# Kernel optimization log

Measured on AMD Instinct MI355X. Metric: run time of the kernel, lower is better.

The kernel has to match this reference:

```python
import jax, jax.numpy as jnp
import numpy as np

# dims
B, L, HID = 2, 1024, 2048
NH, HD, NKV = 32, 64, 8
INTER = 8192
DSSM, MH, MP, MS, MG, MK = 2048, 32, 64, 64, 1, 4
CONV_DIM = DSSM + 2 * MG * MS
EPS = 1e-5
ROPE_BASE = 1e11
# multipliers from config
KEY_MULT, ATTN_IN, ATTN_OUT = 0.7, 1.2, 0.8
SSM_IN, SSM_OUT = 1.1, 0.9
GATE_MULT, DOWN_MULT = 0.9, 0.8
SSM_MULTS = (1.0, 0.9, 0.8, 1.1, 1.2)


def _rms(x, w, eps=EPS):
    return x * jax.lax.rsqrt(jnp.mean(x * x, -1, keepdims=True) + eps) * w


def _rope(pos, x):  # neox-style, full head_dim; x: (B,L,H,HD)
    half = HD // 2
    inv = ROPE_BASE ** (-jnp.arange(0, HD, 2, dtype=jnp.float32) / HD)
    ang = pos.astype(jnp.float32)[:, None] * inv  # (L, half)
    cos = jnp.cos(ang)[None, :, None, :]
    sin = jnp.sin(ang)[None, :, None, :]
    x1, x2 = x[..., :half], x[..., half:]
    return jnp.concatenate([x1 * cos - x2 * sin, x2 * cos + x1 * sin], -1)


def _mup_vector():
    return jnp.concatenate([
        jnp.full((DSSM,), SSM_MULTS[0], jnp.float32),
        jnp.full((DSSM,), SSM_MULTS[1], jnp.float32),
        jnp.full((MG * MS,), SSM_MULTS[2], jnp.float32),
        jnp.full((MG * MS,), SSM_MULTS[3], jnp.float32),
        jnp.full((MH,), SSM_MULTS[4], jnp.float32),
    ])


def setup_inputs() -> dict:
    key = jax.random.key(0)
    ks = jax.random.split(key, 16)
    s = 0.02
    return {
        "hidden_states": jax.random.normal(ks[0], (B, L, HID), jnp.float32),
        "positions": jnp.arange(L, dtype=jnp.int32),
        "w_in_ln": jnp.ones((HID,), jnp.float32),
        "qkv_w": jax.random.normal(ks[1], (NH * HD + 2 * NKV * HD, HID), jnp.float32) * s,
        "o_w": jax.random.normal(ks[2], (HID, NH * HD), jnp.float32) * s,
        "in_proj_w": jax.random.normal(ks[3], (2 * DSSM + 2 * MG * MS + MH, HID), jnp.float32) * s,
        "conv_w": jax.random.normal(ks[4], (CONV_DIM, MK), jnp.float32) * 0.1,
        "conv_b": jax.random.normal(ks[5], (CONV_DIM,), jnp.float32) * 0.01,
        "A_log": jnp.log(jnp.linspace(1.0, 16.0, MH, dtype=jnp.float32)),
        "dt_bias": jax.random.normal(ks[6], (MH,), jnp.float32) * 0.1,
        "D": jnp.ones((MH,), jnp.float32),
        "ssm_norm_w": jnp.ones((DSSM,), jnp.float32),
        "out_proj_w": jax.random.normal(ks[7], (HID, DSSM), jnp.float32) * s,
        "w_pre_ff_ln": jnp.ones((HID,), jnp.float32),
        "gate_up_w": jax.random.normal(ks[8], (2 * INTER, HID), jnp.float32) * s,
        "down_w": jax.random.normal(ks[9], (HID, INTER), jnp.float32) * s,
    }


def _attention(hs, positions, qkv_w, o_w):
    qkv = hs @ qkv_w.T
    qs, kvs = NH * HD, NKV * HD
    q = qkv[..., :qs].reshape(B, L, NH, HD)
    k = qkv[..., qs:qs + kvs].reshape(B, L, NKV, HD) * KEY_MULT
    v = qkv[..., qs + kvs:].reshape(B, L, NKV, HD)
    q = _rope(positions, q)
    k = _rope(positions, k)
    rep = NH // NKV
    qg = q.reshape(B, L, NKV, rep, HD)
    scores = jnp.einsum('blgrd,bmgd->bgrlm', qg, k) * (HD ** -0.5)
    mask = jnp.tril(jnp.ones((L, L), bool))
    scores = jnp.where(mask[None, None, None], scores, jnp.float32(-1e9))
    attn = jax.nn.softmax(scores, axis=-1)
    out = jnp.einsum('bgrlm,bmgd->blgrd', attn, v).reshape(B, L, NH * HD)
    return out @ o_w.T


def _mamba(hs, in_proj_w, conv_w, conv_b, A_log, dt_bias, D, ssm_norm_w, out_proj_w):
    proj = (hs @ in_proj_w.T) * _mup_vector()  # (B,L,2*DSSM+2*G*S+MH)
    z = proj[..., :DSSM]
    xBC = proj[..., DSSM:DSSM + CONV_DIM]
    dt = proj[..., -MH:]
    # causal depthwise conv1d, kernel MK, then silu
    xpad = jnp.pad(xBC, ((0, 0), (MK - 1, 0), (0, 0)))
    conv = sum(xpad[:, k:k + L, :] * conv_w[:, k] for k in range(MK)) + conv_b
    xBC = jax.nn.silu(conv)
    x = xBC[..., :DSSM].reshape(B, L, MH, MP)
    Bm = xBC[..., DSSM:DSSM + MG * MS].reshape(B, L, MS)  # G=1
    C = xBC[..., DSSM + MG * MS:].reshape(B, L, MS)
    dt = jax.nn.softplus(dt + dt_bias)  # (B,L,MH)
    A = -jnp.exp(A_log)  # (MH,)

    def step(state, inp):  # state: (B,MH,MP,MS)
        x_t, dt_t, b_t, c_t = inp  # (B,MH,MP),(B,MH),(B,MS),(B,MS)
        dA = jnp.exp(dt_t * A)  # (B,MH)
        dBx = dt_t[..., None, None] * x_t[..., None] * b_t[:, None, None, :]
        state = state * dA[..., None, None] + dBx
        y = jnp.einsum('bhps,bs->bhp', state, c_t)
        return state, y

    xs = (jnp.moveaxis(x, 1, 0), jnp.moveaxis(dt, 1, 0),
          jnp.moveaxis(Bm, 1, 0), jnp.moveaxis(C, 1, 0))
    state0 = jnp.zeros((B, MH, MP, MS), hs.dtype)
    _, ys = jax.lax.scan(step, state0, xs)
    y = jnp.moveaxis(ys, 0, 1) + x * D[None, None, :, None]  # (B,L,MH,MP)
    y = y.reshape(B, L, DSSM)
    # gated RMSNorm: gate with silu(z), then rms-normalize
    g = y * jax.nn.silu(z)
    g = _rms(g, ssm_norm_w)
    return g @ out_proj_w.T


def _mlp(x, gate_up_w, down_w):
    gu = x @ gate_up_w.T
    gate = gu[..., :INTER] * GATE_MULT
    up = gu[..., INTER:]
    return (jax.nn.silu(gate) * up) @ down_w.T * DOWN_MULT


def reference(hidden_states, positions, w_in_ln, qkv_w, o_w, in_proj_w, conv_w,
              conv_b, A_log, dt_bias, D, ssm_norm_w, out_proj_w, w_pre_ff_ln,
              gate_up_w, down_w):
    residual = hidden_states
    hs = _rms(hidden_states, w_in_ln)
    attn_h = _attention(hs * ATTN_IN, positions, qkv_w, o_w)
    ssm_h = _mamba(hs * SSM_IN, in_proj_w, conv_w, conv_b, A_log, dt_bias, D,
                   ssm_norm_w, out_proj_w)
    h = attn_h * ATTN_OUT + ssm_h * SSM_OUT + residual
    residual = h
    h = _rms(h, w_pre_ff_ln)
    h = _mlp(h, gate_up_w, down_w)
    return h + residual
```

## Files before the change

### kernel.cpp

```cpp
#include <hip/hip_runtime.h>
#include <hip/hip_bf16.h>
#include <math.h>

#define B_      2
#define L_      1024
#define HID     2048
#define T_      (B_*L_)
#define NH      32
#define HD      64
#define NKV     8
#define INTER   8192
#define DSSM    2048
#define MH      32
#define MP      64
#define MS      64
#define MK      4
#define CONV_DIM 2176
#define QKV_N   3072
#define INPROJ_N 4256
#define CH      16
#define CL      64

typedef __bf16 bf16x8 __attribute__((ext_vector_type(8)));
typedef __bf16 bf16x4 __attribute__((ext_vector_type(4)));
typedef float  floatx4 __attribute__((ext_vector_type(4)));

static const size_t OFF_H2   = 0;
static const size_t OFF_MUP  = 4194304;
static const size_t AR       = 4210688;
static const size_t OFF_WQKV = AR;
static const size_t OFF_WIN  = OFF_WQKV + 3145728;
static const size_t OFF_WO   = OFF_WIN  + 4358144;
static const size_t OFF_WOP  = OFF_WO   + 2097152;
static const size_t OFF_HSB  = OFF_WOP  + 2097152;
static const size_t OFF_HSF  = OFF_HSB  + 2097152;
static const size_t OFF_QKV  = OFF_HSF  + 4194304;
static const size_t OFF_Q    = OFF_QKV  + 6291456;
static const size_t OFF_K    = OFF_Q    + 2097152;
static const size_t OFF_V    = OFF_K    + 524288;
static const size_t OFF_ATT  = OFF_V    + 524288;
static const size_t OFF_PROJ = OFF_ATT  + 2097152;
static const size_t OFF_XBC  = OFF_PROJ + 8716288;
static const size_t OFF_Y    = OFF_XBC  + 4456448;
static const size_t OFF_G    = OFF_Y    + 4194304;
static const size_t OFF_TB   = OFF_QKV;
static const size_t OFF_DEC  = OFF_Q;
static const size_t OFF_LAM  = OFF_V;
static const size_t OFF_HS2B = AR;
static const size_t OFF_GU   = AR + 2097152;
static const size_t OFF_ACTB = OFF_GU + 33554432;
static const size_t OFF_WB2  = OFF_ACTB + 8388608;

__device__ inline float block_sum(float v, float* red) {
#pragma unroll
  for (int o = 32; o > 0; o >>= 1) v += __shfl_down(v, o, 64);
  const int lane = threadIdx.x & 63, wv = threadIdx.x >> 6;
  if (lane == 0) red[wv] = v;
  __syncthreads();
  if (threadIdx.x == 0) red[0] = red[0] + red[1] + red[2] + red[3];
  __syncthreads();
  float r = red[0];
  __syncthreads();
  return r;
}

__device__ inline bf16x8 pack8(float4 a, float4 b, float scale) {
  bf16x8 v;
  v[0] = (__bf16)(a.x * scale); v[1] = (__bf16)(a.y * scale);
  v[2] = (__bf16)(a.z * scale); v[3] = (__bf16)(a.w * scale);
  v[4] = (__bf16)(b.x * scale); v[5] = (__bf16)(b.y * scale);
  v[6] = (__bf16)(b.z * scale); v[7] = (__bf16)(b.w * scale);
  return v;
}

__device__ __forceinline__ void async16(const void* g, void* l) {
  __builtin_amdgcn_global_load_lds(
      (const __attribute__((address_space(1))) void*)g,
      (__attribute__((address_space(3))) void*)l, 16, 0, 0);
}

__global__ __launch_bounds__(256) void cvt_kernel(
    const float* __restrict__ in, __bf16* __restrict__ outp, int n8)
{
  int i = blockIdx.x * 256 + threadIdx.x;
  const int stride = gridDim.x * 256;
  for (; i < n8; i += stride) {
    const float4* p = (const float4*)(in + (size_t)i * 8);
    float4 a = p[0], b = p[1];
    bf16x8 v;
    v[0] = (__bf16)a.x; v[1] = (__bf16)a.y; v[2] = (__bf16)a.z; v[3] = (__bf16)a.w;
    v[4] = (__bf16)b.x; v[5] = (__bf16)b.y; v[6] = (__bf16)b.z; v[7] = (__bf16)b.w;
    *(bf16x8*)(outp + (size_t)i * 8) = v;
  }
}

__global__ __launch_bounds__(256) void copy_kernel(
    const float* __restrict__ in, float* __restrict__ outp)
{
  const size_t i = ((size_t)blockIdx.x * 256 + threadIdx.x) * 4;
  *(float4*)&outp[i] = *(const float4*)&in[i];
}

__global__ __launch_bounds__(256) void gemm_bf_kernel(
    const __bf16* __restrict__ A, const __bf16* __restrict__ W,
    float* __restrict__ out, const float* __restrict__ addin,
    const float* __restrict__ colscale,
    int N, int K, int ldo, float alpha)
{
  __shared__ __align__(16) __bf16 As[128 * 32];
  __shared__ __align__(16) __bf16 Bs[128 * 32];
  const int tid = threadIdx.x;
  const int lane = tid & 63, wave = tid >> 6;
  const int fr = lane & 15, fq = lane >> 4;
  const int m0 = blockIdx.x * 128, n0 = blockIdx.y * 128;
  const int wm = (wave >> 1) * 64, wn = (wave & 1) * 64;

  const int KS = K / gridDim.z;
  const int kbase = blockIdx.z * KS;

  const int srow = wave * 32 + (lane >> 2);
  const int selem = (lane & 3) * 8;
  const __bf16* ga0 = A + (size_t)(m0 + srow) * K + kbase + selem;
  const __bf16* ga1 = ga0 + (size_t)16 * K;
  int wr0 = n0 + srow;      if (wr0 >= N) wr0 = N - 1;
  int wr1 = n0 + srow + 16; if (wr1 >= N) wr1 = N - 1;
  const __bf16* gb0 = W + (size_t)wr0 * K + kbase + selem;
  const __bf16* gb1 = W + (size_t)wr1 * K + kbase + selem;
  __bf16* lA0 = &As[(wave * 2 + 0) * 512];
  __bf16* lA1 = &As[(wave * 2 + 1) * 512];
  __bf16* lB0 = &Bs[(wave * 2 + 0) * 512];
  __bf16* lB1 = &Bs[(wave * 2 + 1) * 512];

  floatx4 acc[4][4];
#pragma unroll
  for (int i = 0; i < 4; i++)
#pragma unroll
    for (int j = 0; j < 4; j++) acc[i][j] = (floatx4){0.f, 0.f, 0.f, 0.f};

  for (int kk = 0; kk < KS; kk += 32) {
    async16(ga0, lA0); async16(ga1, lA1);
    async16(gb0, lB0); async16(gb1, lB1);
    ga0 += 32; ga1 += 32; gb0 += 32; gb1 += 32;
    __syncthreads();

    bf16x8 aF[4], bF[4];
#pragma unroll
    for (int i = 0; i < 4; i++)
      aF[i] = *(const bf16x8*)&As[(wm + i * 16 + fr) * 32 + fq * 8];
#pragma unroll
    for (int j = 0; j < 4; j++)
      bF[j] = *(const bf16x8*)&Bs[(wn + j * 16 + fr) * 32 + fq * 8];
#pragma unroll
    for (int i = 0; i < 4; i++)
#pragma unroll
      for (int j = 0; j < 4; j++)
        acc[i][j] = __builtin_amdgcn_mfma_f32_16x16x32_bf16(aF[i], bF[j], acc[i][j], 0, 0, 0);
    __syncthreads();
  }

  const bool at = (gridDim.z > 1);
#pragma unroll
  for (int i = 0; i < 4; i++) {
#pragma unroll
    for (int r = 0; r < 4; r++) {
      const int m = m0 + wm + i * 16 + fq * 4 + r;
      float* orow = out + (size_t)m * ldo;
      const float* arow = addin ? (addin + (size_t)m * ldo) : nullptr;
#pragma unroll
      for (int j = 0; j < 4; j++) {
        const int n = n0 + wn + j * 16 + fr;
        if (n < N) {
          float vv = acc[i][j][r] * alpha;
          if (colscale) vv *= colscale[n];
          if (at) {
            atomicAdd(&orow[n], vv);
          } else {
            if (arow) vv += arow[n];
            orow[n] = vv;
          }
        }
      }
    }
  }
}

__global__ __launch_bounds__(256) void rms_kernel(
    const float* __restrict__ in, const float* __restrict__ w,
    __bf16* __restrict__ outb, float* __restrict__ outf, float* __restrict__ copy)
{
  __shared__ float buf[HID];
  __shared__ float red[8];
  const int tid = threadIdx.x;
  const size_t t = blockIdx.x;
  const float* row = in + t * HID;
  float ss = 0.f;
  for (int i = tid; i < HID; i += 256) { float x = row[i]; buf[i] = x; ss += x * x; }
  float tot = block_sum(ss, red);
  float inv = rsqrtf(tot / (float)HID + 1e-5f);
  for (int i = tid; i < HID; i += 256) {
    float x = buf[i];
    float val = x * inv * w[i];
    outb[t * HID + i] = (__bf16)val;
    if (outf) outf[t * HID + i] = val;
    if (copy) copy[t * HID + i] = x;
  }
}

__global__ void mup_kernel(float* __restrict__ mup) {
  int i = blockIdx.x * 256 + threadIdx.x;
  if (i >= INPROJ_N) return;
  float v = (i < DSSM) ? 1.0f
          : (i < 2 * DSSM) ? 0.9f
          : (i < 2 * DSSM + MS) ? 0.8f
          : (i < 2 * DSSM + 2 * MS) ? 1.1f
          : 1.2f;
  mup[i] = v;
}

__global__ __launch_bounds__(256) void rope_kernel(
    const float* __restrict__ qkv, const int* __restrict__ positions,
    __bf16* __restrict__ q, __bf16* __restrict__ k, __bf16* __restrict__ v)
{
  __shared__ float inv_s[32];
  const int tid = threadIdx.x;
  const size_t t = blockIdx.x;
  const int l = (int)(t & (L_ - 1));
  if (tid < 32) inv_s[tid] = powf(1.0e11f, -(float)(2 * tid) / 64.f);
  __syncthreads();
  const float pos = (float)positions[l];
  const float* src = qkv + t * QKV_N;
  for (int idx = tid; idx < 1536; idx += 256) {
    int head = idx >> 5, hd = idx & 31;
    if (head < 32) {
      float ang = pos * inv_s[hd];
      float c = cosf(ang), sn = sinf(ang);
      float x1 = src[head * 64 + hd], x2 = src[head * 64 + 32 + hd];
      __bf16* dst = q + (t * NH + head) * HD;
      dst[hd] = (__bf16)((x1 * c - x2 * sn) * 0.125f);
      dst[hd + 32] = (__bf16)((x2 * c + x1 * sn) * 0.125f);
    } else if (head < 40) {
      int kk = head - 32;
      float ang = pos * inv_s[hd];
      float c = cosf(ang), sn = sinf(ang);
      float x1 = src[2048 + kk * 64 + hd] * 0.7f;
      float x2 = src[2048 + kk * 64 + 32 + hd] * 0.7f;
      __bf16* dst = k + (t * NKV + kk) * HD;
      dst[hd] = (__bf16)(x1 * c - x2 * sn);
      dst[hd + 32] = (__bf16)(x2 * c + x1 * sn);
    } else {
      int vv = head - 40;
      __bf16* dst = v + (t * NKV + vv) * HD;
      dst[hd] = (__bf16)src[2560 + vv * 64 + hd];
      dst[hd + 32] = (__bf16)src[2560 + vv * 64 + 32 + hd];
    }
  }
}

__global__ __launch_bounds__(256) void fattn_kernel(
    const __bf16* __restrict__ q, const __bf16* __restrict__ k,
    const __bf16* __restrict__ v, __bf16* __restrict__ out)
{
  __shared__ __align__(16) __bf16 Vt[64][72];
  __shared__ __align__(16) __bf16 Ps[4][16][72];
  const int tid = threadIdx.x;
  const int wave = tid >> 6, lane = tid & 63;
  const int fr = lane & 15, fq = lane >> 4;
  const int qt = (int)(gridDim.x - 1) - blockIdx.x;
  const int h = blockIdx.y, b = blockIdx.z, g = h >> 2;
  const int l0 = qt * 64;

  bf16x8 qf[2];
  {
    const int qrow = l0 + wave * 16 + fr;
    const __bf16* qp = q + (((size_t)(b * L_ + qrow)) * NH + h) * HD;
    qf[0] = *(const bf16x8*)&qp[fq * 8];
    qf[1] = *(const bf16x8*)&qp[32 + fq * 8];
  }

  floatx4 O[4];
  float m_run[4], l_run[4];
#pragma unroll
  for (int i = 0; i < 4; i++) { O[i] = (floatx4){0.f,0.f,0.f,0.f}; m_run[i] = -3.0e38f; l_run[i] = 0.f; }

  for (int kt = 0; kt <= qt; kt++) {
    __syncthreads();
#pragma unroll
    for (int pp = 0; pp < 4; pp++) {
      const int kb = pp * 4 + wave;
      bf16x4 pk;
#pragma unroll
      for (int c = 0; c < 4; c++)
        pk[c] = v[(((size_t)(b * L_ + kt * 64 + kb * 4 + c)) * NKV + g) * HD + lane];
      *(bf16x4*)&Vt[lane][kb * 4] = pk;
    }

    floatx4 S[4];
#pragma unroll
    for (int j = 0; j < 4; j++) {
      const __bf16* kp = k + (((size_t)(b * L_ + kt * 64 + j * 16 + fr)) * NKV + g) * HD;
      floatx4 sa = (floatx4){0.f,0.f,0.f,0.f};
#pragma unroll
      for (int s = 0; s < 2; s++) {
        bf16x8 kf = *(const bf16x8*)&kp[s * 32 + fq * 8];
        sa = __builtin_amdgcn_mfma_f32_16x16x32_bf16(qf[s], kf, sa, 0, 0, 0);
      }
      S[j] = sa;
    }

    if (kt == qt) {
      const int qbase = wave * 16 + fq * 4;
#pragma unroll
      for (int j = 0; j < 4; j++)
#pragma unroll
        for (int r = 0; r < 4; r++)
          if (j * 16 + fr > qbase + r) S[j][r] = -1.0e30f;
    }

    float rm[4], alpha[4], rsum[4];
#pragma unroll
    for (int r = 0; r < 4; r++)
      rm[r] = fmaxf(fmaxf(S[0][r], S[1][r]), fmaxf(S[2][r], S[3][r]));
#pragma unroll
    for (int msk = 1; msk <= 8; msk <<= 1)
#pragma unroll
      for (int r = 0; r < 4; r++) rm[r] = fmaxf(rm[r], __shfl_xor(rm[r], msk, 64));
#pragma unroll
    for (int r = 0; r < 4; r++) {
      float mnew = fmaxf(m_run[r], rm[r]);
      alpha[r] = __expf(m_run[r] - mnew);
      m_run[r] = mnew;
    }
#pragma unroll
    for (int j = 0; j < 4; j++)
#pragma unroll
      for (int r = 0; r < 4; r++) S[j][r] = __expf(S[j][r] - m_run[r]);
#pragma unroll
    for (int r = 0; r < 4; r++)
      rsum[r] = S[0][r] + S[1][r] + S[2][r] + S[3][r];
#pragma unroll
    for (int msk = 1; msk <= 8; msk <<= 1)
#pragma unroll
      for (int r = 0; r < 4; r++) rsum[r] += __shfl_xor(rsum[r], msk, 64);
#pragma unroll
    for (int r = 0; r < 4; r++) l_run[r] = l_run[r] * alpha[r] + rsum[r];
#pragma unroll
    for (int d4 = 0; d4 < 4; d4++)
#pragma unroll
      for (int r = 0; r < 4; r++) O[d4][r] *= alpha[r];

#pragma unroll
    for (int j = 0; j < 4; j++)
#pragma unroll
      for (int r = 0; r < 4; r++)
        Ps[wave][fq * 4 + r][j * 16 + fr] = (__bf16)S[j][r];

    __syncthreads();

#pragma unroll
    for (int s = 0; s < 2; s++) {
      bf16x8 pf = *(const bf16x8*)&Ps[wave][fr][s * 32 + fq * 8];
#pragma unroll
      for (int d4 = 0; d4 < 4; d4++) {
        bf16x8 vf = *(const bf16x8*)&Vt[d4 * 16 + fr][s * 32 + fq * 8];
        O[d4] = __builtin_amdgcn_mfma_f32_16x16x32_bf16(pf, vf, O[d4], 0, 0, 0);
      }
    }
  }

  float rl[4];
#pragma unroll
  for (int r = 0; r < 4; r++) rl[r] = 1.f / l_run[r];
#pragma unroll
  for (int d4 = 0; d4 < 4; d4++)
#pragma unroll
    for (int r = 0; r < 4; r++) {
      const int qg = l0 + wave * 16 + fq * 4 + r;
      out[((size_t)(b * L_ + qg)) * HID + h * 64 + d4 * 16 + fr] = (__bf16)(O[d4][r] * rl[r]);
    }
}

__global__ __launch_bounds__(256) void dtfix_kernel(
    const float* __restrict__ hs_ln, const float* __restrict__ w, float* __restrict__ proj)
{
  const size_t t = blockIdx.x;
  const int tid = threadIdx.x;
  const int o = tid >> 3, part = tid & 7;
  const float* a = hs_ln + t * HID;
  const float* wr = w + (size_t)(INPROJ_N - MH + o) * HID;
  float s = 0.f;
  for (int kk = part * 4; kk < HID; kk += 32) {
    const float4 av = *(const float4*)&a[kk];
    const float4 wv = *(const float4*)&wr[kk];
    s += av.x * wv.x + av.y * wv.y + av.z * wv.z + av.w * wv.w;
  }
  s += __shfl_xor(s, 1);
  s += __shfl_xor(s, 2);
  s += __shfl_xor(s, 4);
  if (part == 0) proj[t * INPROJ_N + (INPROJ_N - MH) + o] = s * 1.32f;
}

__global__ __launch_bounds__(256) void conv_kernel(
    const float* __restrict__ proj, const float* __restrict__ cw,
    const float* __restrict__ cb, float* __restrict__ xbc)
{
  const int c = blockIdx.x * 256 + threadIdx.x;
  if (c >= CONV_DIM) return;
  const int t = blockIdx.y;
  const int l = t & (L_ - 1);
  float acc = cb[c];
#pragma unroll
  for (int kk = 0; kk < MK; kk++) {
    int lp = l - (MK - 1) + kk;
    if (lp >= 0)
      acc += proj[((size_t)(t - (MK - 1) + kk)) * INPROJ_N + DSSM + c] * cw[c * MK + kk];
  }
  xbc[(size_t)t * CONV_DIM + c] = acc / (1.f + __expf(-acc));
}

__global__ __launch_bounds__(256) void scanA_kernel(
    const float* __restrict__ xbc, const float* __restrict__ proj,
    const float* __restrict__ A_log, const float* __restrict__ dt_bias,
    const float* __restrict__ Dp,
    float* __restrict__ y, float* __restrict__ Tbuf,
    float* __restrict__ lam, float* __restrict__ dec)
{
  __shared__ __align__(16) __bf16 xT[64][72];
  __shared__ __align__(16) __bf16 BTw[64][72];
  __shared__ __align__(16) __bf16 Braw[64][72];
  __shared__ __align__(16) __bf16 Craw[64][72];
  __shared__ __align__(16) __bf16 Ps[4][16][72];
  __shared__ float dt_s[64], cum_s[64];

  const int tid = threadIdx.x;
  const int lane = tid & 63, wave = tid >> 6;
  const int fr = lane & 15, fq = lane >> 4;
  const int c = blockIdx.x, h = blockIdx.y, b = blockIdx.z;
  const int t0 = b * L_ + c * CL;
  const float Ah = -expf(A_log[h]);
  const float dtb = dt_bias[h], Dh = Dp[h];

  if (wave == 0) {
    float draw = proj[(size_t)(t0 + lane) * INPROJ_N + (INPROJ_N - MH) + h];
    float dtv = draw + dtb;
    dtv = (dtv > 20.f) ? dtv : log1pf(__expf(dtv));
    float cs = dtv * Ah;
#pragma unroll
    for (int d = 1; d < 64; d <<= 1) {
      float nv = __shfl_up(cs, d, 64);
      if (lane >= d) cs += nv;
    }
    dt_s[lane] = dtv;
    cum_s[lane] = cs;
  }

#pragma unroll
  for (int pass = 0; pass < 4; pass++) {
    const int l = pass * 16 + (tid >> 4);
    const int s4 = (tid & 15) * 4;
    const float* rowp = xbc + (size_t)(t0 + l) * CONV_DIM;
    float4 xv = *(const float4*)&rowp[h * 64 + s4];
    float4 bv = *(const float4*)&rowp[DSSM + s4];
    float4 cv = *(const float4*)&rowp[DSSM + MS + s4];
    xT[s4 + 0][l] = (__bf16)xv.x;
    xT[s4 + 1][l] = (__bf16)xv.y;
    xT[s4 + 2][l] = (__bf16)xv.z;
    xT[s4 + 3][l] = (__bf16)xv.w;
    bf16x4 b4; b4[0]=(__bf16)bv.x; b4[1]=(__bf16)bv.y; b4[2]=(__bf16)bv.z; b4[3]=(__bf16)bv.w;
    *(bf16x4*)&Braw[l][s4] = b4;
    bf16x4 c4; c4[0]=(__bf16)cv.x; c4[1]=(__bf16)cv.y; c4[2]=(__bf16)cv.z; c4[3]=(__bf16)cv.w;
    *(bf16x4*)&Craw[l][s4] = c4;
  }
  __syncthreads();

  const float cend = cum_s[63];
#pragma unroll
  for (int pass = 0; pass < 4; pass++) {
    const int l = pass * 16 + (tid >> 4);
    const int s4 = (tid & 15) * 4;
    const float wl = __expf(cend - cum_s[l]) * dt_s[l];
    float4 bv = *(const float4*)&xbc[(size_t)(t0 + l) * CONV_DIM + DSSM + s4];
    BTw[s4 + 0][l] = (__bf16)(bv.x * wl);
    BTw[s4 + 1][l] = (__bf16)(bv.y * wl);
    BTw[s4 + 2][l] = (__bf16)(bv.z * wl);
    BTw[s4 + 3][l] = (__bf16)(bv.w * wl);
  }

  {
    bf16x8 aF0 = *(const bf16x8*)&Craw[wave * 16 + fr][fq * 8];
    bf16x8 aF1 = *(const bf16x8*)&Craw[wave * 16 + fr][fq * 8 + 32];
#pragma unroll
    for (int j = 0; j < 4; j++) {
      floatx4 s = (floatx4){0.f,0.f,0.f,0.f};
      bf16x8 b0 = *(const bf16x8*)&Braw[j * 16 + fr][fq * 8];
      bf16x8 b1 = *(const bf16x8*)&Braw[j * 16 + fr][fq * 8 + 32];
      s = __builtin_amdgcn_mfma_f32_16x16x32_bf16(aF0, b0, s, 0, 0, 0);
      s = __builtin_amdgcn_mfma_f32_16x16x32_bf16(aF1, b1, s, 0, 0, 0);
      const int m = j * 16 + fr;
      const float dtm = dt_s[m], cmm = cum_s[m];
#pragma unroll
      for (int r = 0; r < 4; r++) {
        const int lR = wave * 16 + fq * 4 + r;
        float f = (m <= lR) ? __expf(cum_s[lR] - cmm) * dtm : 0.f;
        Ps[wave][fq * 4 + r][m] = (__bf16)(s[r] * f);
      }
    }
  }
  __syncthreads();

  {
    bf16x8 aF0 = *(const bf16x8*)&Ps[wave][fr][fq * 8];
    bf16x8 aF1 = *(const bf16x8*)&Ps[wave][fr][fq * 8 + 32];
#pragma unroll
    for (int j = 0; j < 4; j++) {
      floatx4 s = (floatx4){0.f,0.f,0.f,0.f};
      bf16x8 b0 = *(const bf16x8*)&xT[j * 16 + fr][fq * 8];
      bf16x8 b1 = *(const bf16x8*)&xT[j * 16 + fr][fq * 8 + 32];
      s = __builtin_amdgcn_mfma_f32_16x16x32_bf16(aF0, b0, s, 0, 0, 0);
      s = __builtin_amdgcn_mfma_f32_16x16x32_bf16(aF1, b1, s, 0, 0, 0);
      const int p = j * 16 + fr;
#pragma unroll
      for (int r = 0; r < 4; r++) {
        const int lR = wave * 16 + fq * 4 + r;
        float xval = (float)xT[p][lR];
        y[(size_t)(t0 + lR) * DSSM + h * 64 + p] = s[r] + Dh * xval;
      }
    }
  }

  {
    float* Tb = Tbuf + ((size_t)((b * MH + h) * CH + c)) * 4096;
    bf16x8 aF0 = *(const bf16x8*)&xT[wave * 16 + fr][fq * 8];
    bf16x8 aF1 = *(const bf16x8*)&xT[wave * 16 + fr][fq * 8 + 32];
#pragma unroll
    for (int j = 0; j < 4; j++) {
      floatx4 s = (floatx4){0.f,0.f,0.f,0.f};
      bf16x8 b0 = *(const bf16x8*)&BTw[j * 16 + fr][fq * 8];
      bf16x8 b1 = *(const bf16x8*)&BTw[j * 16 + fr][fq * 8 + 32];
      s = __builtin_amdgcn_mfma_f32_16x16x32_bf16(aF0, b0, s, 0, 0, 0);
      s = __builtin_amdgcn_mfma_f32_16x16x32_bf16(aF1, b1, s, 0, 0, 0);
#pragma unroll
      for (int r = 0; r < 4; r++)
        Tb[(wave * 16 + fq * 4 + r) * 64 + j * 16 + fr] = s[r];
    }
  }

  if (tid == 0) lam[(b * MH + h) * CH + c] = __expf(cend);
  if (tid >= 64 && tid < 128)
    dec[((size_t)((b * MH + h) * CH + c)) * 64 + (tid - 64)] = __expf(cum_s[tid - 64]);
}

__global__ __launch_bounds__(256) void scanB_kernel(
    const float* __restrict__ xbc, const float* __restrict__ Tbuf,
    const float* __restrict__ lam, const float* __restrict__ dec,
    float* __restrict__ y)
{
  __shared__ __align__(16) float S[64][68];
  __shared__ __align__(16) __bf16 Cc[64][72];
  __shared__ float decl[64];
  const int tid = threadIdx.x;
  const int lane = tid & 63, wave = tid >> 6;
  const int fr = lane & 15, fq = lane >> 4;
  const int h = blockIdx.x, b = blockIdx.y;

  const int sown = tid & 63, pbase = (tid >> 6) * 16;
#pragma unroll
  for (int i = 0; i < 16; i++) S[pbase + i][sown] = 0.f;
  __syncthreads();

  for (int c = 0; c < CH; c++) {
    const int t0 = b * L_ + c * CL;
#pragma unroll
    for (int pass = 0; pass < 4; pass++) {
      const int l = pass * 16 + (tid >> 4);
      const int s4 = (tid & 15) * 4;
      float4 cv = *(const float4*)&xbc[(size_t)(t0 + l) * CONV_DIM + DSSM + MS + s4];
      bf16x4 c4; c4[0]=(__bf16)cv.x; c4[1]=(__bf16)cv.y; c4[2]=(__bf16)cv.z; c4[3]=(__bf16)cv.w;
      *(bf16x4*)&Cc[l][s4] = c4;
    }
    if (tid < 64) decl[tid] = dec[((size_t)((b * MH + h) * CH + c)) * 64 + tid];
    __syncthreads();

    if (c > 0) {
      bf16x8 aF0 = *(const bf16x8*)&Cc[wave * 16 + fr][fq * 8];
      bf16x8 aF1 = *(const bf16x8*)&Cc[wave * 16 + fr][fq * 8 + 32];
#pragma unroll
      for (int j = 0; j < 4; j++) {
        const float* srow = &S[j * 16 + fr][0];
        float4 s0 = *(const float4*)&srow[fq * 8];
        float4 s1 = *(const float4*)&srow[fq * 8 + 4];
        float4 s2 = *(const float4*)&srow[fq * 8 + 32];
        float4 s3 = *(const float4*)&srow[fq * 8 + 36];
        bf16x8 b0 = pack8(s0, s1, 1.f);
        bf16x8 b1 = pack8(s2, s3, 1.f);
        floatx4 acc = (floatx4){0.f,0.f,0.f,0.f};
        acc = __builtin_amdgcn_mfma_f32_16x16x32_bf16(aF0, b0, acc, 0, 0, 0);
        acc = __builtin_amdgcn_mfma_f32_16x16x32_bf16(aF1, b1, acc, 0, 0, 0);
        const int p = j * 16 + fr;
#pragma unroll
        for (int r = 0; r < 4; r++) {
          const int lR = wave * 16 + fq * 4 + r;
          float* yp = &y[(size_t)(t0 + lR) * DSSM + h * 64 + p];
          *yp += decl[lR] * acc[r];
        }
      }
    }
    __syncthreads();

    const float lc = lam[(b * MH + h) * CH + c];
    const float* Tb = Tbuf + ((size_t)((b * MH + h) * CH + c)) * 4096;
#pragma unroll
    for (int i = 0; i < 16; i++) {
      float tv = Tb[(pbase + i) * 64 + sown];
      S[pbase + i][sown] = lc * S[pbase + i][sown] + tv;
    }
    __syncthreads();
  }
}

__global__ __launch_bounds__(256) void gating_kernel(
    const float* __restrict__ y, const float* __restrict__ proj,
    const float* __restrict__ nw, __bf16* __restrict__ g)
{
  __shared__ float buf[DSSM];
  __shared__ float red[8];
  const int tid = threadIdx.x;
  const size_t t = blockIdx.x;
  float ss = 0.f;
  for (int i = tid; i < DSSM; i += 256) {
    float zv = proj[t * INPROJ_N + i];
    float yv = y[t * DSSM + i];
    float gv = yv * zv / (1.f + __expf(-zv));
    buf[i] = gv;
    ss += gv * gv;
  }
  float tot = block_sum(ss, red);
  float inv = rsqrtf(tot / (float)DSSM + 1e-5f);
  for (int i = tid; i < DSSM; i += 256) g[t * DSSM + i] = (__bf16)(buf[i] * inv * nw[i]);
}

__global__ __launch_bounds__(256) void act_kernel(
    const float* __restrict__ gu, __bf16* __restrict__ act)
{
  const int i = (blockIdx.x * 256 + threadIdx.x) * 4;
  const size_t t = blockIdx.y;
  float4 g4 = *(const float4*)&gu[t * (2 * INTER) + i];
  float4 u4 = *(const float4*)&gu[t * (2 * INTER) + INTER + i];
  bf16x4 o;
  float gt;
  gt = g4.x * 0.9f; o[0] = (__bf16)(gt / (1.f + __expf(-gt)) * u4.x);
  gt = g4.y * 0.9f; o[1] = (__bf16)(gt / (1.f + __expf(-gt)) * u4.y);
  gt = g4.z * 0.9f; o[2] = (__bf16)(gt / (1.f + __expf(-gt)) * u4.z);
  gt = g4.w * 0.9f; o[3] = (__bf16)(gt / (1.f + __expf(-gt)) * u4.w);
  *(bf16x4*)&act[t * INTER + i] = o;
}

extern "C" void kernel_launch(void* const* d_in, const int* in_sizes, int n_in,
                              void* d_out, int out_size, void* d_ws, size_t ws_size,
                              hipStream_t stream)
{
  const float* hidden      = (const float*)d_in[0];
  const int*   positions   = (const int*)d_in[1];
  const float* w_in_ln     = (const float*)d_in[2];
  const float* qkv_w       = (const float*)d_in[3];
  const float* o_w         = (const float*)d_in[4];
  const float* in_proj_w   = (const float*)d_in[5];
  const float* conv_w      = (const float*)d_in[6];
  const float* conv_b      = (const float*)d_in[7];
  const float* A_log       = (const float*)d_in[8];
  const float* dt_bias     = (const float*)d_in[9];
  const float* Dp          = (const float*)d_in[10];
  const float* ssm_norm_w  = (const float*)d_in[11];
  const float* out_proj_w  = (const float*)d_in[12];
  const float* w_pre_ff_ln = (const float*)d_in[13];
  const float* gate_up_w   = (const float*)d_in[14];
  const float* down_w      = (const float*)d_in[15];
  (void)in_sizes; (void)n_in; (void)out_size; (void)ws_size;

  float* ws   = (float*)d_ws;
  float* outp = (float*)d_out;

  float*  h2    = ws + OFF_H2;
  float*  mup   = ws + OFF_MUP;
  __bf16* wqkv  = (__bf16*)(ws + OFF_WQKV);
  __bf16* win   = (__bf16*)(ws + OFF_WIN);
  __bf16* wo    = (__bf16*)(ws + OFF_WO);
  __bf16* wop   = (__bf16*)(ws + OFF_WOP);
  __bf16* hsb   = (__bf16*)(ws + OFF_HSB);
  float*  hsf   = ws + OFF_HSF;
  float*  qkv   = ws + OFF_QKV;
  __bf16* qb    = (__bf16*)(ws + OFF_Q);
  __bf16* kb    = (__bf16*)(ws + OFF_K);
  __bf16* vb    = (__bf16*)(ws + OFF_V);
  __bf16* attb  = (__bf16*)(ws + OFF_ATT);
  float*  proj  = ws + OFF_PROJ;
  float*  xbc   = ws + OFF_XBC;
  float*  y     = ws + OFF_Y;
  __bf16* gb    = (__bf16*)(ws + OFF_G);
  float*  Tbuf  = ws + OFF_TB;
  float*  dec   = ws + OFF_DEC;
  float*  lam   = ws + OFF_LAM;
  __bf16* hs2b  = (__bf16*)(ws + OFF_HS2B);
  float*  gu    = ws + OFF_GU;
  __bf16* actb  = (__bf16*)(ws + OFF_ACTB);
  __bf16* wb2   = (__bf16*)(ws + OFF_WB2);

  cvt_kernel<<<2048, 256, 0, stream>>>(qkv_w, wqkv, 786432);
  cvt_kernel<<<2048, 256, 0, stream>>>(in_proj_w, win, 1089536);
  cvt_kernel<<<2048, 256, 0, stream>>>(o_w, wo, 524288);
  cvt_kernel<<<2048, 256, 0, stream>>>(out_proj_w, wop, 524288);
  mup_kernel<<<17, 256, 0, stream>>>(mup);
  rms_kernel<<<T_, 256, 0, stream>>>(hidden, w_in_ln, hsb, hsf, h2);

  gemm_bf_kernel<<<dim3(16, 24, 1), 256, 0, stream>>>(hsb, wqkv, qkv, nullptr, nullptr,
                                                      QKV_N, HID, QKV_N, 1.2f);
  rope_kernel<<<T_, 256, 0, stream>>>(qkv, positions, qb, kb, vb);
  fattn_kernel<<<dim3(L_ / 64, NH, B_), 256, 0, stream>>>(qb, kb, vb, attb);
  gemm_bf_kernel<<<dim3(16, 16, 4), 256, 0, stream>>>(attb, wo, h2, nullptr, nullptr,
                                                      HID, HID, HID, 0.8f);

  gemm_bf_kernel<<<dim3(16, 34, 1), 256, 0, stream>>>(hsb, win, proj, nullptr, mup,
                                                      INPROJ_N, HID, INPROJ_N, 1.1f);
  dtfix_kernel<<<T_, 256, 0, stream>>>(hsf, in_proj_w, proj);
  conv_kernel<<<dim3(9, T_), 256, 0, stream>>>(proj, conv_w, conv_b, xbc);
  scanA_kernel<<<dim3(CH, MH, B_), 256, 0, stream>>>(xbc, proj, A_log, dt_bias, Dp,
                                                     y, Tbuf, lam, dec);
  scanB_kernel<<<dim3(MH, B_), 256, 0, stream>>>(xbc, Tbuf, lam, dec, y);
  gating_kernel<<<T_, 256, 0, stream>>>(y, proj, ssm_norm_w, gb);
  gemm_bf_kernel<<<dim3(16, 16, 4), 256, 0, stream>>>(gb, wop, h2, nullptr, nullptr,
                                                      HID, HID, HID, 0.9f);

  rms_kernel<<<T_, 256, 0, stream>>>(h2, w_pre_ff_ln, hs2b, nullptr, nullptr);
  cvt_kernel<<<2048, 256, 0, stream>>>(gate_up_w, wb2, 2097152);
  gemm_bf_kernel<<<dim3(16, 64, 1), 256, 0, stream>>>(hs2b, wb2, gu, nullptr, nullptr,
                                                      INTER, HID, 2 * INTER, 1.0f);
  cvt_kernel<<<2048, 256, 0, stream>>>(gate_up_w + (size_t)INTER * HID, wb2, 2097152);
  gemm_bf_kernel<<<dim3(16, 64, 1), 256, 0, stream>>>(hs2b, wb2, gu + INTER, nullptr, nullptr,
                                                      INTER, HID, 2 * INTER, 1.0f);
  act_kernel<<<dim3(INTER / 1024, T_), 256, 0, stream>>>(gu, actb);
  cvt_kernel<<<2048, 256, 0, stream>>>(down_w, wb2, 2097152);
  copy_kernel<<<4096, 256, 0, stream>>>(h2, outp);
  gemm_bf_kernel<<<dim3(16, 16, 4), 256, 0, stream>>>(actb, wb2, outp, nullptr, nullptr,
                                                      HID, INTER, HID, 0.8f);
}
```

Baseline: 1.283 ms.

## Double-buffer LDS tiles in bf16 GEMM and remap workgroups across XCDs

The GEMM now keeps two shared-memory stages so the async global-to-LDS load of the next K tile is issued before the MFMA work on the current tile, with one barrier per step instead of two. It also remaps the linear workgroup id so consecutive blocks are spread over the eight chiplets and M tiles are grouped, which is meant to improve L2 reuse. The remap hardcodes 16 M tiles (M=2048) and assumes the block count divides by 8. LDS use doubles.

```diff
diff --git a/kernel.cpp b/kernel.cpp
--- a/kernel.cpp
+++ b/kernel.cpp
@@ -107,16 +107,21 @@
     const float* __restrict__ colscale,
     int N, int K, int ldo, float alpha)
 {
-  __shared__ __align__(16) __bf16 As[128 * 32];
-  __shared__ __align__(16) __bf16 Bs[128 * 32];
+  __shared__ __align__(16) __bf16 As[2][128 * 32];
+  __shared__ __align__(16) __bf16 Bs[2][128 * 32];
   const int tid = threadIdx.x;
   const int lane = tid & 63, wave = tid >> 6;
   const int fr = lane & 15, fq = lane >> 4;
-  const int m0 = blockIdx.x * 128, n0 = blockIdx.y * 128;
+
+  const int nwg = (int)(gridDim.x * gridDim.y);
+  int lid = (int)(blockIdx.y * gridDim.x + blockIdx.x);
+  lid = (lid & 7) * (nwg >> 3) + (lid >> 3);
+  const int m0 = (lid & 15) * 128;
+  const int n0 = (lid >> 4) * 128;
   const int wm = (wave >> 1) * 64, wn = (wave & 1) * 64;
 
   const int KS = K / gridDim.z;
-  const int kbase = blockIdx.z * KS;
+  const int kbase = (int)blockIdx.z * KS;
 
   const int srow = wave * 32 + (lane >> 2);
   const int selem = (lane & 3) * 8;
@@ -126,10 +131,7 @@
   int wr1 = n0 + srow + 16; if (wr1 >= N) wr1 = N - 1;
   const __bf16* gb0 = W + (size_t)wr0 * K + kbase + selem;
   const __bf16* gb1 = W + (size_t)wr1 * K + kbase + selem;
-  __bf16* lA0 = &As[(wave * 2 + 0) * 512];
-  __bf16* lA1 = &As[(wave * 2 + 1) * 512];
-  __bf16* lB0 = &Bs[(wave * 2 + 0) * 512];
-  __bf16* lB1 = &Bs[(wave * 2 + 1) * 512];
+  const int sbase = wave * 2 * 512;
 
   floatx4 acc[4][4];
 #pragma unroll
@@ -137,25 +139,48 @@
 #pragma unroll
     for (int j = 0; j < 4; j++) acc[i][j] = (floatx4){0.f, 0.f, 0.f, 0.f};
 
-  for (int kk = 0; kk < KS; kk += 32) {
-    async16(ga0, lA0); async16(ga1, lA1);
-    async16(gb0, lB0); async16(gb1, lB1);
+  async16(ga0, &As[0][sbase]); async16(ga1, &As[0][sbase + 512]);
+  async16(gb0, &Bs[0][sbase]); async16(gb1, &Bs[0][sbase + 512]);
+  ga0 += 32; ga1 += 32; gb0 += 32; gb1 += 32;
+  __syncthreads();
+
+  const int nsteps = KS >> 5;
+  int cur = 0;
+  for (int s = 0; s < nsteps - 1; ++s) {
+    async16(ga0, &As[cur ^ 1][sbase]); async16(ga1, &As[cur ^ 1][sbase + 512]);
+    async16(gb0, &Bs[cur ^ 1][sbase]); async16(gb1, &Bs[cur ^ 1][sbase + 512]);
     ga0 += 32; ga1 += 32; gb0 += 32; gb1 += 32;
-    __syncthreads();
 
     bf16x8 aF[4], bF[4];
 #pragma unroll
     for (int i = 0; i < 4; i++)
-      aF[i] = *(const bf16x8*)&As[(wm + i * 16 + fr) * 32 + fq * 8];
+      aF[i] = *(const bf16x8*)&As[cur][(wm + i * 16 + fr) * 32 + fq * 8];
 #pragma unroll
     for (int j = 0; j < 4; j++)
-      bF[j] = *(const bf16x8*)&Bs[(wn + j * 16 + fr) * 32 + fq * 8];
+      bF[j] = *(const bf16x8*)&Bs[cur][(wn + j * 16 + fr) * 32 + fq * 8];
 #pragma unroll
     for (int i = 0; i < 4; i++)
 #pragma unroll
       for (int j = 0; j < 4; j++)
         acc[i][j] = __builtin_amdgcn_mfma_f32_16x16x32_bf16(aF[i], bF[j], acc[i][j], 0, 0, 0);
+
     __syncthreads();
+    cur ^= 1;
+  }
+
+  {
+    bf16x8 aF[4], bF[4];
+#pragma unroll
+    for (int i = 0; i < 4; i++)
+      aF[i] = *(const bf16x8*)&As[cur][(wm + i * 16 + fr) * 32 + fq * 8];
+#pragma unroll
+    for (int j = 0; j < 4; j++)
+      bF[j] = *(const bf16x8*)&Bs[cur][(wn + j * 16 + fr) * 32 + fq * 8];
+#pragma unroll
+    for (int i = 0; i < 4; i++)
+#pragma unroll
+      for (int j = 0; j < 4; j++)
+        acc[i][j] = __builtin_amdgcn_mfma_f32_16x16x32_bf16(aF[i], bF[j], acc[i][j], 0, 0, 0);
   }
 
   const bool at = (gridDim.z > 1);
```

New measurement: 1.265 ms. No clear change (-1.4%).
